# Kernel tuning notes

Measured on AMD Instinct MI355X. Metric: run time of the kernel, lower is better.

## Reference

```python
import jax, jax.numpy as jnp
import numpy as np

B, S, HID, NH = 1, 2048, 2048, 16
HD = HID // NH
HALF = HD // 2
# quantization scales (registered buffers / pack() scales in the original module)
ATTN_IN_SCALE = 0.02   # attn_input_scale: dequant scale of int8 hidden_states
Q_OUT_SCALE = 0.05     # q_output_scale
K_OUT_SCALE = 0.05     # k_output_scale
V_OUT_SCALE = 0.04     # v_output_scale
Q_ROT_SCALE = 0.06     # q_rotary_output_scale
K_ROT_SCALE = 0.06     # k_rotary_output_scale
OUT_IN_SCALE = 0.03    # out_input_scale
W_ALPHA = 0.002        # folded int8 GEMM alpha for q/k/v W8A8B8O8Linear
BETA = 1.0             # bias scale of W8A8B8O8Linear
O_ALPHA = 0.001        # folded alpha for o_proj W8A8BFP32OFP32Linear
PROB_SCALE = 1.0 / 127.0  # attention-prob int8 quant scale
INV_SQRT_HD = float(1.0 / np.sqrt(HD))


def _q8(x):
    # saturating int8 quantization (values kept in float32)
    return jnp.clip(jnp.round(x), -127.0, 127.0)


def setup_inputs() -> dict:
    key = jax.random.key(0)
    ks = jax.random.split(key, 10)
    hidden_states = jax.random.normal(ks[0], (B, S, HID), jnp.float32)
    pos = jnp.arange(S, dtype=jnp.float32)
    inv_freq = 1.0 / (10000.0 ** (jnp.arange(0, HD, 2, dtype=jnp.float32) / HD))
    freqs = pos[:, None] * inv_freq[None, :]          # (S, HD//2)
    cos, sin = jnp.cos(freqs), jnp.sin(freqs)
    w8 = lambda k: jax.random.randint(k, (HID, HID), -127, 128).astype(jnp.float32)
    b8 = lambda k: jax.random.randint(k, (HID,), -127, 128).astype(jnp.float32)
    return dict(
        hidden_states=hidden_states, cos=cos, sin=sin,
        wq=w8(ks[1]), wk=w8(ks[2]), wv=w8(ks[3]), wo=w8(ks[4]),
        bq=b8(ks[5]), bk=b8(ks[6]), bv=b8(ks[7]),
        bo=jax.random.normal(ks[8], (HID,), jnp.float32) * 0.01,
    )


def reference(hidden_states, cos, sin, wq, wk, wv, wo, bq, bk, bv, bo):
    # quantize activations to int8 (done upstream of the module in smoothquant)
    x8 = _q8(hidden_states / ATTN_IN_SCALE)                       # (B,S,HID) int8 vals

    # W8A8B8O8Linear: int8 GEMM, alpha-scaled, int8 bias, saturate to int8
    def lin8(x, w, b):
        return _q8(jnp.einsum('bsi,oi->bso', x, w) * W_ALPHA + BETA * b)

    q8, k8, v8 = lin8(x8, wq, bq), lin8(x8, wk, bk), lin8(x8, wv, bv)

    # int8_rotary_embedding_fwd: dequant -> split-half rotary -> requant
    def rope(x8_flat, in_scale, out_scale):
        x = x8_flat.reshape(B, S, NH, HD) * in_scale
        x0, x1 = x[..., :HALF], x[..., HALF:]
        c, s_ = cos[None, :, None, :], sin[None, :, None, :]
        rot = jnp.concatenate([x0 * c - x1 * s_, x0 * s_ + x1 * c], axis=-1)
        return _q8(rot / out_scale)

    q = rope(q8, Q_OUT_SCALE, Q_ROT_SCALE)                        # (B,S,NH,HD)
    k = rope(k8, K_OUT_SCALE, K_ROT_SCALE)
    v = v8.reshape(B, S, NH, HD)

    # smooth_llama_context_attn_fwd: int8 QK^T -> fp32 scores -> causal softmax
    scores = jnp.einsum('bqhd,bkhd->bhqk', q, k) * (Q_ROT_SCALE * K_ROT_SCALE * INV_SQRT_HD)
    causal = jnp.tril(jnp.ones((S, S), bool))
    scores = jnp.where(causal[None, None], scores, -1e9)
    p = jax.nn.softmax(scores, axis=-1)
    p8 = _q8(p * 127.0)                                           # quantize probs to int8
    # int8 PV bmm, rescale and saturate to int8 for o_proj input
    o8 = _q8(jnp.einsum('bhqk,bkhd->bqhd', p8, v) * (PROB_SCALE * V_OUT_SCALE / OUT_IN_SCALE))
    o8 = o8.reshape(B, S, HID)

    # W8A8BFP32OFP32Linear: int8 GEMM, fp32 alpha + fp32 bias
    out = jnp.einsum('bso,po->bsp', o8, wo) * O_ALPHA + bo
    return out
```

## Files before the change

### kernel.cpp

```cpp
#include <hip/hip_runtime.h>
#include <math.h>

typedef __attribute__((ext_vector_type(4))) int i32x4;
typedef signed char s8;

constexpr int S   = 2048;
constexpr int HID = 2048;
constexpr int NH  = 16;
constexpr int HD  = 128;
constexpr int HALF = 64;

#define SCORE_SCALE ((float)(0.06 * 0.06 * 0.08838834764831845))
#define OSCALE      ((float)(((1.0 / 127.0) * 0.04) / 0.03))

__device__ __forceinline__ float clip127(float r){
  return fminf(fmaxf(r, -127.0f), 127.0f);
}
__device__ __forceinline__ i32x4 mfma_i8(i32x4 a, i32x4 b, i32x4 c){
  return __builtin_amdgcn_mfma_i32_16x16x64_i8(a, b, c, 0, 0, 0);
}
__device__ __forceinline__ void async16(const void* g, void* l){
  __builtin_amdgcn_global_load_lds(
      (const __attribute__((address_space(1))) unsigned*)g,
      (__attribute__((address_space(3))) unsigned*)l, 16, 0, 0);
}
template<int ROWS>
__device__ __forceinline__ void stage_async_swz(s8* dst, const s8* src, int stride){
  const int tid = threadIdx.x;
#pragma unroll
  for (int i = 0; i < ROWS/32; ++i){
    int o = i*256 + tid;
    int row = o >> 3, ch = o & 7;
    async16(src + (size_t)row*stride + ((ch ^ (row & 7))*16), dst + o*16);
  }
}
__device__ __forceinline__ i32x4 rd16(const s8* buf, int row, int ch){
  return *(const i32x4*)(buf + row*128 + ((ch ^ (row & 7))*16));
}
__device__ __forceinline__ int tri_qt(int t){
  int qt = (int)((sqrtf(8.f*t + 1.f) - 1.f)*0.5f);
  while ((qt+1)*(qt+2)/2 <= t) ++qt;
  while (qt*(qt+1)/2 > t) --qt;
  return qt;
}

__global__ void cvt_all(const float* __restrict__ hid, const float* __restrict__ wq,
                        const float* __restrict__ wk, const float* __restrict__ wv,
                        const float* __restrict__ wo, s8* __restrict__ xd,
                        s8* __restrict__ qd, s8* __restrict__ kd,
                        s8* __restrict__ vd, s8* __restrict__ od, int n){
  const float* srcs[5] = {hid, wq, wk, wv, wo};
  s8* dsts[5] = {xd, qd, kd, vd, od};
  int which = blockIdx.y;
  const float* src = srcs[which];
  s8* dst = dsts[which];
  int i = (blockIdx.x * blockDim.x + threadIdx.x) * 4;
  if (i >= n) return;
  float4 v = *(const float4*)(src + i);
  float x[4] = {v.x, v.y, v.z, v.w};
  unsigned packed = 0;
#pragma unroll
  for (int j = 0; j < 4; ++j){
    int b;
    if (which == 0) b = (int)clip127(rintf(x[j] / 0.02f));
    else            b = (int)x[j];
    packed |= ((unsigned)(b & 255)) << (8*j);
  }
  *(unsigned*)(dst + i) = packed;
}

__global__ __launch_bounds__(256)
void gemm_qkv(const s8* __restrict__ A, const s8* __restrict__ W,
              const float* __restrict__ bq, const float* __restrict__ bk,
              const float* __restrict__ bv, s8* __restrict__ Out){
#pragma clang fp contract(off)
  constexpr int Kd = 2048, N = 2048;
  const int z = blockIdx.z;
  const s8* Bt = W + (size_t)z*(4u<<20);
  s8* Y = Out + (size_t)z*(4u<<20);
  const float* bss[3] = {bq, bk, bv};
  const float* bias = bss[z];
  __shared__ __attribute__((aligned(16))) s8 As[128*128];
  __shared__ __attribute__((aligned(16))) s8 Bs[128*128];
  const int bm = blockIdx.x, bn = blockIdx.y, tid = threadIdx.x;
  const int wid = tid >> 6, lane = tid & 63;
  const int wm = wid >> 1, wn = wid & 1;
  const int col16 = lane & 15, g = lane >> 4;
  i32x4 acc[4][4] = {};
  const s8* Ab = A + (size_t)(bm*128)*Kd;
  const s8* Bb = Bt + (size_t)(bn*128)*Kd;
  for (int kt = 0; kt < 16; ++kt){
    stage_async_swz<128>(As, Ab + kt*128, Kd);
    stage_async_swz<128>(Bs, Bb + kt*128, Kd);
    __syncthreads();
#pragma unroll
    for (int kk = 0; kk < 2; ++kk){
      i32x4 af[4], bf[4];
#pragma unroll
      for (int i = 0; i < 4; ++i) af[i] = rd16(As, wm*64 + i*16 + col16, kk*4 + g);
#pragma unroll
      for (int j = 0; j < 4; ++j) bf[j] = rd16(Bs, wn*64 + j*16 + col16, kk*4 + g);
#pragma unroll
      for (int i = 0; i < 4; ++i)
#pragma unroll
        for (int j = 0; j < 4; ++j)
          acc[i][j] = mfma_i8(af[i], bf[j], acc[i][j]);
    }
    __syncthreads();
  }
#pragma unroll
  for (int i = 0; i < 4; ++i){
#pragma unroll
    for (int j = 0; j < 4; ++j){
      int row0 = bm*128 + wm*64 + i*16 + g*4;
      int col  = bn*128 + wn*64 + j*16 + col16;
#pragma unroll
      for (int r = 0; r < 4; ++r){
        float t = (float)acc[i][j][r] * 0.002f;
        t = t + bias[col];
        Y[(size_t)(row0 + r)*N + col] = (s8)(int)clip127(rintf(t));
      }
    }
  }
}

__global__ __launch_bounds__(256)
void gemm_o(const s8* __restrict__ A, const s8* __restrict__ Bt,
            const float* __restrict__ bias, float* __restrict__ Y){
#pragma clang fp contract(off)
  constexpr int Kd = 2048, N = 2048;
  __shared__ __attribute__((aligned(16))) s8 As[128*128];
  __shared__ __attribute__((aligned(16))) s8 Bs[64*128];
  const int bm = blockIdx.x, bn = blockIdx.y, tid = threadIdx.x;
  const int wid = tid >> 6, lane = tid & 63;
  const int wm = wid >> 1, wn = wid & 1;
  const int col16 = lane & 15, g = lane >> 4;
  i32x4 acc[4][2] = {};
  const s8* Ab = A + (size_t)(bm*128)*Kd;
  const s8* Bb = Bt + (size_t)(bn*64)*Kd;
  for (int kt = 0; kt < 16; ++kt){
    stage_async_swz<128>(As, Ab + kt*128, Kd);
    stage_async_swz<64>(Bs, Bb + kt*128, Kd);
    __syncthreads();
#pragma unroll
    for (int kk = 0; kk < 2; ++kk){
      i32x4 af[4], bf[2];
#pragma unroll
      for (int i = 0; i < 4; ++i) af[i] = rd16(As, wm*64 + i*16 + col16, kk*4 + g);
#pragma unroll
      for (int j = 0; j < 2; ++j) bf[j] = rd16(Bs, wn*32 + j*16 + col16, kk*4 + g);
#pragma unroll
      for (int i = 0; i < 4; ++i)
#pragma unroll
        for (int j = 0; j < 2; ++j)
          acc[i][j] = mfma_i8(af[i], bf[j], acc[i][j]);
    }
    __syncthreads();
  }
#pragma unroll
  for (int i = 0; i < 4; ++i){
#pragma unroll
    for (int j = 0; j < 2; ++j){
      int row0 = bm*128 + wm*64 + i*16 + g*4;
      int col  = bn*64 + wn*32 + j*16 + col16;
#pragma unroll
      for (int r = 0; r < 4; ++r){
        float t = (float)acc[i][j][r] * 0.001f;
        t = t + bias[col];
        Y[(size_t)(row0 + r)*N + col] = t;
      }
    }
  }
}

__global__ void rope_qk(s8* __restrict__ q, s8* __restrict__ k,
                        const float* __restrict__ cosp, const float* __restrict__ sinp){
#pragma clang fp contract(off)
  int idx = blockIdx.x * blockDim.x + threadIdx.x;
  int t4 = (idx & 15) * 4;
  int h  = (idx >> 4) & (NH-1);
  int s  = idx >> 8;
  if (s >= S) return;
  float4 c4 = *(const float4*)(cosp + s*HALF + t4);
  float4 s4 = *(const float4*)(sinp + s*HALF + t4);
  float cc[4] = {c4.x, c4.y, c4.z, c4.w}, ss[4] = {s4.x, s4.y, s4.z, s4.w};
  int base = s*HID + h*HD + t4;
  {
    int a0 = *(const int*)(q + base), a1 = *(const int*)(q + base + HALF);
    unsigned o0 = 0, o1 = 0;
#pragma unroll
    for (int j = 0; j < 4; ++j){
      float x0 = (float)((s8)(a0 >> (8*j))) * 0.05f;
      float x1 = (float)((s8)(a1 >> (8*j))) * 0.05f;
      float r0 = x0*cc[j] - x1*ss[j];
      float r1 = x0*ss[j] + x1*cc[j];
      o0 |= ((unsigned)(((int)clip127(rintf(r0 / 0.06f))) & 255)) << (8*j);
      o1 |= ((unsigned)(((int)clip127(rintf(r1 / 0.06f))) & 255)) << (8*j);
    }
    *(unsigned*)(q + base) = o0; *(unsigned*)(q + base + HALF) = o1;
  }
  {
    int a0 = *(const int*)(k + base), a1 = *(const int*)(k + base + HALF);
    unsigned o0 = 0, o1 = 0;
#pragma unroll
    for (int j = 0; j < 4; ++j){
      float x0 = (float)((s8)(a0 >> (8*j))) * 0.05f;
      float x1 = (float)((s8)(a1 >> (8*j))) * 0.05f;
      float r0 = x0*cc[j] - x1*ss[j];
      float r1 = x0*ss[j] + x1*cc[j];
      o0 |= ((unsigned)(((int)clip127(rintf(r0 / 0.06f))) & 255)) << (8*j);
      o1 |= ((unsigned)(((int)clip127(rintf(r1 / 0.06f))) & 255)) << (8*j);
    }
    *(unsigned*)(k + base) = o0; *(unsigned*)(k + base + HALF) = o1;
  }
}

__global__ void vtrans(const s8* __restrict__ v, s8* __restrict__ vt){
  __shared__ __attribute__((aligned(16))) s8 t[128*144];
  int s0 = blockIdx.x * 128, h = blockIdx.y;
  int tid = threadIdx.x;
#pragma unroll
  for (int i = 0; i < 4; ++i){
    int vv = i*256 + tid, r = vv >> 3, ch = vv & 7;
    *(i32x4*)(t + r*144 + ch*16) = *(const i32x4*)(v + (size_t)(s0 + r)*HID + h*HD + ch*16);
  }
  __syncthreads();
#pragma unroll
  for (int i = 0; i < 4; ++i){
    int vv = i*256 + tid, d = vv >> 3, sc = (vv & 7)*16;
    s8 tmp[16];
#pragma unroll
    for (int j = 0; j < 16; ++j) tmp[j] = t[(sc + j)*144 + d];
    *(i32x4*)(vt + (size_t)(h*HD + d)*S + s0 + sc) = *(i32x4*)tmp;
  }
}

__global__ __launch_bounds__(256)
void attn_stats(const s8* __restrict__ qr, const s8* __restrict__ kr,
                float2* __restrict__ stats){
  const int x = blockIdx.x, h = blockIdx.y;
  const int tri = x >> 1, half = x & 1;
  const int qt = tri_qt(tri);
  const int kt = tri - qt*(qt+1)/2;
  const int q0 = qt*128 + half*64;
  const int tid = threadIdx.x, wid = tid >> 6, lane = tid & 63;
  const int col16 = lane & 15, g = lane >> 4;
  __shared__ __attribute__((aligned(16))) s8 Ks[128*128];

  stage_async_swz<128>(Ks, kr + (size_t)(kt*128)*HID + h*HD, HID);
  const s8* qb = qr + (size_t)(q0 + wid*16 + col16)*HID + h*HD + g*16;
  i32x4 aq[2];
  aq[0] = *(const i32x4*)(qb);
  aq[1] = *(const i32x4*)(qb + 64);
  __syncthreads();

  i32x4 sc[8] = {};
#pragma unroll
  for (int kk = 0; kk < 2; ++kk){
#pragma unroll
    for (int j = 0; j < 8; ++j){
      i32x4 bk = rd16(Ks, j*16 + col16, kk*4 + g);
      sc[j] = mfma_i8(aq[kk], bk, sc[j]);
    }
  }

  const bool diag = (kt == qt);
#pragma unroll
  for (int r = 0; r < 4; ++r){
    int rit = half*64 + wid*16 + g*4 + r;
    int qrow = qt*128 + rit;
    int mi = (int)0x80000000;
#pragma unroll
    for (int j = 0; j < 8; ++j){
      int v = sc[j][r];
      if (diag && (kt*128 + j*16 + col16 > qrow)) v = (int)0x80000000;
      mi = max(mi, v);
    }
    mi = max(mi, __shfl_xor(mi, 1));
    mi = max(mi, __shfl_xor(mi, 2));
    mi = max(mi, __shfl_xor(mi, 4));
    mi = max(mi, __shfl_xor(mi, 8));
    float mf = (float)mi * SCORE_SCALE;
    float st = 0.f;
#pragma unroll
    for (int j = 0; j < 8; ++j){
      float arg;
      if (diag && (kt*128 + j*16 + col16 > qrow)) arg = -1e30f;
      else arg = (float)sc[j][r] * SCORE_SCALE - mf;
      st += __expf(arg);
    }
    st += __shfl_xor(st, 1);
    st += __shfl_xor(st, 2);
    st += __shfl_xor(st, 4);
    st += __shfl_xor(st, 8);
    if (col16 == 0) stats[(size_t)(h*136 + tri)*128 + rit] = make_float2(mf, st);
  }
}

__global__ void attn_reduce(const float2* __restrict__ stats, float2* __restrict__ ml){
  const int row = threadIdx.x, qt = blockIdx.x, h = blockIdx.y;
  const int tri = qt*(qt+1)/2;
  float m = -3.0e38f;
  for (int kt = 0; kt <= qt; ++kt)
    m = fmaxf(m, stats[(size_t)(h*136 + tri + kt)*128 + row].x);
  float l = 0.f;
  for (int kt = 0; kt <= qt; ++kt){
    float2 s = stats[(size_t)(h*136 + tri + kt)*128 + row];
    l += s.y * __expf(s.x - m);
  }
  ml[(h*16 + qt)*128 + row] = make_float2(m, l);
}

__global__ __launch_bounds__(256)
void attn_score(const s8* __restrict__ qr, const s8* __restrict__ kr,
                const float2* __restrict__ ml, s8* __restrict__ P8){
  const int x = blockIdx.x, h = blockIdx.y;
  const int tri = x >> 1, half = x & 1;
  const int qt = tri_qt(tri);
  const int kt = tri - qt*(qt+1)/2;
  const int q0 = qt*128 + half*64;
  const int tid = threadIdx.x, wid = tid >> 6, lane = tid & 63;
  const int col16 = lane & 15, g = lane >> 4;
  __shared__ __attribute__((aligned(16))) s8 Ks[128*128];
  __shared__ __attribute__((aligned(16))) s8 Pl[64*128];

  stage_async_swz<128>(Ks, kr + (size_t)(kt*128)*HID + h*HD, HID);
  const s8* qb = qr + (size_t)(q0 + wid*16 + col16)*HID + h*HD + g*16;
  i32x4 aq[2];
  aq[0] = *(const i32x4*)(qb);
  aq[1] = *(const i32x4*)(qb + 64);
  float m[4], c[4];
#pragma unroll
  for (int r = 0; r < 4; ++r){
    float2 t = ml[(h*16 + qt)*128 + half*64 + wid*16 + g*4 + r];
    m[r] = t.x;
    c[r] = 127.0f / t.y;
  }
  __syncthreads();

  const bool diag = (kt == qt);
#pragma unroll
  for (int j = 0; j < 8; ++j){
    i32x4 s0 = {};
    s0 = mfma_i8(aq[0], rd16(Ks, j*16 + col16, g), s0);
    s0 = mfma_i8(aq[1], rd16(Ks, j*16 + col16, 4 + g), s0);
    int colk = j*16 + col16;
#pragma unroll
    for (int r = 0; r < 4; ++r){
      int row = wid*16 + g*4 + r;
      int qrow = q0 + row;
      float p8v = 0.0f;
      if (!diag || (kt*128 + colk) <= qrow){
        float sv = (float)s0[r] * SCORE_SCALE;
        p8v = clip127(rintf(__expf(sv - m[r]) * c[r]));
      }
      Pl[row*128 + colk] = (s8)(int)p8v;
    }
  }
  __syncthreads();
  s8* dst = P8 + (size_t)(h*136 + tri)*16384 + half*8192;
#pragma unroll
  for (int i = 0; i < 2; ++i){
    int o = i*256 + tid;
    *(i32x4*)(dst + o*16) = *(const i32x4*)(Pl + o*16);
  }
}

__global__ __launch_bounds__(256)
void attn_pv(const s8* __restrict__ P8, const s8* __restrict__ vt8,
             s8* __restrict__ o8){
  const int qt = 15 - blockIdx.x;
  const int h = blockIdx.y, dh = blockIdx.z;
  const int tri = qt*(qt+1)/2;
  const int tid = threadIdx.x, wid = tid >> 6, lane = tid & 63;
  const int wm = wid >> 1, wn = wid & 1;
  const int col16 = lane & 15, g = lane >> 4;
  __shared__ __attribute__((aligned(16))) s8 Ps[128*128];
  __shared__ __attribute__((aligned(16))) s8 Vs[64*128];

  i32x4 acc[4][2] = {};
  for (int kt = 0; kt <= qt; ++kt){
    stage_async_swz<128>(Ps, P8 + (size_t)(h*136 + tri + kt)*16384, 128);
    stage_async_swz<64>(Vs, vt8 + (size_t)(h*HD + dh*64)*S + kt*128, S);
    __syncthreads();
#pragma unroll
    for (int kk = 0; kk < 2; ++kk){
      i32x4 af[4], bf[2];
#pragma unroll
      for (int i = 0; i < 4; ++i) af[i] = rd16(Ps, wm*64 + i*16 + col16, kk*4 + g);
#pragma unroll
      for (int j = 0; j < 2; ++j) bf[j] = rd16(Vs, wn*32 + j*16 + col16, kk*4 + g);
#pragma unroll
      for (int i = 0; i < 4; ++i)
#pragma unroll
        for (int j = 0; j < 2; ++j)
          acc[i][j] = mfma_i8(af[i], bf[j], acc[i][j]);
    }
    __syncthreads();
  }
#pragma unroll
  for (int i = 0; i < 4; ++i)
#pragma unroll
    for (int j = 0; j < 2; ++j)
#pragma unroll
      for (int r = 0; r < 4; ++r){
        int row = qt*128 + wm*64 + i*16 + g*4 + r;
        int d = dh*64 + wn*32 + j*16 + col16;
        o8[(size_t)row*HID + h*HD + d] = (s8)(int)clip127(rintf((float)acc[i][j][r] * OSCALE));
      }
}

extern "C" void kernel_launch(void* const* d_in, const int* in_sizes, int n_in,
                              void* d_out, int out_size, void* d_ws, size_t ws_size,
                              hipStream_t stream) {
  const float* hidden = (const float*)d_in[0];
  const float* cosp   = (const float*)d_in[1];
  const float* sinp   = (const float*)d_in[2];
  const float* wq     = (const float*)d_in[3];
  const float* wk     = (const float*)d_in[4];
  const float* wv     = (const float*)d_in[5];
  const float* wo     = (const float*)d_in[6];
  const float* bq     = (const float*)d_in[7];
  const float* bk     = (const float*)d_in[8];
  const float* bv     = (const float*)d_in[9];
  const float* bo     = (const float*)d_in[10];
  float* out = (float*)d_out;

  const size_t MB = 1024*1024;
  s8* ws8 = (s8*)d_ws;
  s8* x8  = ws8 + 0*MB;
  s8* wq8 = ws8 + 4*MB;
  s8* wk8 = ws8 + 8*MB;
  s8* wv8 = ws8 + 12*MB;
  s8* wo8 = ws8 + 16*MB;
  s8* q8  = ws8 + 20*MB;
  s8* k8  = ws8 + 24*MB;
  s8* v8  = ws8 + 28*MB;
  s8* vt8 = ws8 + 32*MB;
  s8* P8  = ws8 + 36*MB;
  s8* o8  = x8;
  float2* stats = (float2*)(ws8 + 4*MB);
  float2* mlb   = (float2*)(ws8 + 4*MB + 2400*1024);

  const int n = HID*HID;
  dim3 b256(256);

  cvt_all<<<dim3(n/1024, 5), b256, 0, stream>>>(hidden, wq, wk, wv, wo,
                                                x8, wq8, wk8, wv8, wo8, n);

  gemm_qkv<<<dim3(16, 16, 3), b256, 0, stream>>>(x8, wq8, bq, bk, bv, q8);

  rope_qk<<<(S*NH*16)/256, b256, 0, stream>>>(q8, k8, cosp, sinp);
  vtrans<<<dim3(S/128, NH), b256, 0, stream>>>(v8, vt8);

  attn_stats<<<dim3(272, 16), b256, 0, stream>>>(q8, k8, stats);
  attn_reduce<<<dim3(16, 16), dim3(128), 0, stream>>>(stats, mlb);
  attn_score<<<dim3(272, 16), b256, 0, stream>>>(q8, k8, mlb, P8);
  attn_pv<<<dim3(16, 16, 2), b256, 0, stream>>>(P8, vt8, o8);

  gemm_o<<<dim3(16, 32), b256, 0, stream>>>(o8, wo8, bo, out);
}
```

Measured before the change: 152.7 us.

## Switch QKV GEMM to 32x32x32 int8 MFMA with two-wave 128-thread blocks

Rewrites the QKV projection GEMM to use the larger 32x32x32 int8 MFMA instruction, with each of two waves covering a 64x128 output slab instead of four waves each covering 64x64. Staging is done by 128 threads, and the epilogue follows the 32x32 accumulator layout with the bias loaded once per column. The aim is fewer LDS fragment reads per MFMA and higher per-instruction throughput. In exchange, each block has half the waves, so occupancy and latency hiding drop, and accumulator register pressure rises.

```diff
diff --git a/kernel.cpp b/kernel.cpp
--- a/kernel.cpp
+++ b/kernel.cpp
@@ -2,6 +2,7 @@
 #include <math.h>
 
 typedef __attribute__((ext_vector_type(4))) int i32x4;
+typedef __attribute__((ext_vector_type(16))) int i32x16;
 typedef signed char s8;
 
 constexpr int S   = 2048;
@@ -30,6 +31,15 @@
 #pragma unroll
   for (int i = 0; i < ROWS/32; ++i){
     int o = i*256 + tid;
+    int row = o >> 3, ch = o & 7;
+    async16(src + (size_t)row*stride + ((ch ^ (row & 7))*16), dst + o*16);
+  }
+}
+__device__ __forceinline__ void stage_tile_128thr(s8* dst, const s8* src, int stride){
+  const int tid = threadIdx.x;
+#pragma unroll
+  for (int i = 0; i < 8; ++i){
+    int o = i*128 + tid;
     int row = o >> 3, ch = o & 7;
     async16(src + (size_t)row*stride + ((ch ^ (row & 7))*16), dst + o*16);
   }
@@ -69,7 +79,7 @@
   *(unsigned*)(dst + i) = packed;
 }
 
-__global__ __launch_bounds__(256)
+__global__ __launch_bounds__(128)
 void gemm_qkv(const s8* __restrict__ A, const s8* __restrict__ W,
               const float* __restrict__ bq, const float* __restrict__ bk,
               const float* __restrict__ bv, s8* __restrict__ Out){
@@ -84,41 +94,42 @@
   __shared__ __attribute__((aligned(16))) s8 Bs[128*128];
   const int bm = blockIdx.x, bn = blockIdx.y, tid = threadIdx.x;
   const int wid = tid >> 6, lane = tid & 63;
-  const int wm = wid >> 1, wn = wid & 1;
-  const int col16 = lane & 15, g = lane >> 4;
-  i32x4 acc[4][4] = {};
+  const int l31 = lane & 31, hi = lane >> 5;
+  i32x16 acc[2][4] = {};
   const s8* Ab = A + (size_t)(bm*128)*Kd;
   const s8* Bb = Bt + (size_t)(bn*128)*Kd;
   for (int kt = 0; kt < 16; ++kt){
-    stage_async_swz<128>(As, Ab + kt*128, Kd);
-    stage_async_swz<128>(Bs, Bb + kt*128, Kd);
-    __syncthreads();
-#pragma unroll
-    for (int kk = 0; kk < 2; ++kk){
-      i32x4 af[4], bf[4];
-#pragma unroll
-      for (int i = 0; i < 4; ++i) af[i] = rd16(As, wm*64 + i*16 + col16, kk*4 + g);
-#pragma unroll
-      for (int j = 0; j < 4; ++j) bf[j] = rd16(Bs, wn*64 + j*16 + col16, kk*4 + g);
-#pragma unroll
-      for (int i = 0; i < 4; ++i)
+    stage_tile_128thr(As, Ab + kt*128, Kd);
+    stage_tile_128thr(Bs, Bb + kt*128, Kd);
+    __syncthreads();
+#pragma unroll
+    for (int kk = 0; kk < 4; ++kk){
+      const int ch = kk*2 + hi;
+      i32x4 af[2], bf[4];
+#pragma unroll
+      for (int i = 0; i < 2; ++i) af[i] = rd16(As, wid*64 + i*32 + l31, ch);
+#pragma unroll
+      for (int j = 0; j < 4; ++j) bf[j] = rd16(Bs, j*32 + l31, ch);
+#pragma unroll
+      for (int i = 0; i < 2; ++i)
 #pragma unroll
         for (int j = 0; j < 4; ++j)
-          acc[i][j] = mfma_i8(af[i], bf[j], acc[i][j]);
-    }
-    __syncthreads();
-  }
-#pragma unroll
-  for (int i = 0; i < 4; ++i){
+          acc[i][j] = __builtin_amdgcn_mfma_i32_32x32x32_i8(af[i], bf[j], acc[i][j], 0, 0, 0);
+    }
+    __syncthreads();
+  }
+#pragma unroll
+  for (int i = 0; i < 2; ++i){
 #pragma unroll
     for (int j = 0; j < 4; ++j){
-      int row0 = bm*128 + wm*64 + i*16 + g*4;
-      int col  = bn*128 + wn*64 + j*16 + col16;
-#pragma unroll
-      for (int r = 0; r < 4; ++r){
+      int col = bn*128 + j*32 + l31;
+      float b = bias[col];
+#pragma unroll
+      for (int r = 0; r < 16; ++r){
+        int row = bm*128 + wid*64 + i*32 + (r & 3) + 8*(r >> 2) + 4*hi;
         float t = (float)acc[i][j][r] * 0.002f;
-        t = t + bias[col];
-        Y[(size_t)(row0 + r)*N + col] = (s8)(int)clip127(rintf(t));
+        t = t + b;
+        Y[(size_t)row*N + col] = (s8)(int)clip127(rintf(t));
       }
     }
   }
@@ -448,7 +459,7 @@
   cvt_all<<<dim3(n/1024, 5), b256, 0, stream>>>(hidden, wq, wk, wv, wo,
                                                 x8, wq8, wk8, wv8, wo8, n);
 
-  gemm_qkv<<<dim3(16, 16, 3), b256, 0, stream>>>(x8, wq8, bq, bk, bv, q8);
+  gemm_qkv<<<dim3(16, 16, 3), dim3(128), 0, stream>>>(x8, wq8, bq, bk, bv, q8);
 
   rope_qk<<<(S*NH*16)/256, b256, 0, stream>>>(q8, k8, cosp, sinp);
   vtrans<<<dim3(S/128, NH), b256, 0, stream>>>(v8, vt8);
```

New measurement: 159.1 us. 1.04x slower.
